# Kernel tuning notes

Hardware: AMD Instinct MI355X
Metric: run time of the kernel (lower is better)

Reference implementation:

```python
import jax, jax.numpy as jnp
import numpy as np

F = 128          # feature_size
N = 512          # num_vertices (batch_size fixed to 1 by the original indexing)
C = 32 * 7 * 7 * 7   # 10976, f2 channel dim
G = 13           # f2 spatial grid (indices = (v+1)*6 in [0,12])
EPS = 1e-5


def _block(x, W1, b1, W2, b2, g, be, m, v):
    # Linear -> ELU -> Linear -> ELU -> Dropout(eval=id) -> BatchNorm1d(eval)
    h = jax.nn.elu(x @ W1 + b1)
    h = jax.nn.elu(h @ W2 + b2)
    return (h - m) * (g * jax.lax.rsqrt(v + EPS)) + be


def setup_inputs() -> dict:
    key = jax.random.key(0)
    ks = iter(jax.random.split(key, 80))

    def nrm(sh, s):
        return jax.random.normal(next(ks), sh, jnp.float32) * s

    def lin(i, o):
        return nrm((i, o), 1.0 / np.sqrt(i)), nrm((o,), 0.01)

    def bn():
        g = 1.0 + nrm((F,), 0.05)
        be = nrm((F,), 0.05)
        m = nrm((F,), 0.1)
        v = jax.random.uniform(next(ks), (F,), jnp.float32) + 0.5
        return g, be, m, v

    d = {}
    d['vertices'] = jax.random.uniform(next(ks), (1, N, 3), jnp.float32) * 2.0 - 1.0
    d['f2'] = nrm((1, G, G, G, C), 0.1)
    ii = jnp.arange(N, dtype=jnp.int32)
    d['v1s_idx'] = jnp.repeat(ii, N)   # edge k=(i,j): i = k//N
    d['v2s_idx'] = jnp.tile(ii, N)     #               j = k%N
    d['adj'] = (jax.random.uniform(next(ks), (N, N)) < 0.05).astype(jnp.float32)

    for p, (i, o) in [('mv', (3, F)), ('mf', (C, F)), ('s1', (2 * F, F)),
                      ('s2', (F, F)), ('s3', (2 * F, F))]:
        W1, b1 = lin(i, o)
        W2, b2 = lin(F, F)
        g, be, m, v = bn()
        d.update({p + '_W1': W1, p + '_b1': b1, p + '_W2': W2, p + '_b2': b2,
                  p + '_g': g, p + '_be': be, p + '_m': m, p + '_v': v})
    W3, b3 = lin(F, 2)
    d['s3_W3'], d['s3_b3'] = W3, b3
    return d


def _forward(vertices, f2, adj,
             mv_W1, mv_b1, mv_W2, mv_b2, mv_g, mv_be, mv_m, mv_v,
             mf_W1, mf_b1, mf_W2, mf_b2, mf_g, mf_be, mf_m, mf_v,
             s1_W1, s1_b1, s1_W2, s1_b2, s1_g, s1_be, s1_m, s1_v,
             s2_W1, s2_b1, s2_W2, s2_b2, s2_g, s2_be, s2_m, s2_v,
             s3_W1, s3_b1, s3_W2, s3_b2, s3_g, s3_be, s3_m, s3_v, s3_W3, s3_b3,
             v1s_idx, v2s_idx):
    b, n, _ = vertices.shape
    flat = vertices.reshape(-1, 3)                        # (B*N, 3)
    idx = ((flat + 1.0) * 6.0).astype(jnp.int32)          # grid indices in [0,12]
    f2e = f2[0, idx[:, 0], idx[:, 1], idx[:, 2], :]       # gather: (B*N, C)
    vf = _block(flat, mv_W1, mv_b1, mv_W2, mv_b2, mv_g, mv_be, mv_m, mv_v)
    ff = _block(f2e, mf_W1, mf_b1, mf_W2, mf_b2, mf_g, mf_be, mf_m, mf_v)
    vert = jnp.concatenate([vf, ff], -1).reshape(b, n, 2 * F)  # (B, N, 2F)

    # stage1: NodeToEdge (endpoint combine) -> MLP block over all N^2 edges
    e1 = vert[:, v1s_idx] + vert[:, v2s_idx]              # (B, N*N, 2F)
    s1 = _block(e1, s1_W1, s1_b1, s1_W2, s1_b2, s1_g, s1_be, s1_m, s1_v)  # (B, E, F)

    # stage2: EdgeToNode (adjacency-masked sum) -> MLP -> NodeToEdge
    nodes = jnp.einsum('bijf,ij->bif', s1.reshape(b, n, n, F), adj)  # (B, N, F)
    n2 = _block(nodes, s2_W1, s2_b1, s2_W2, s2_b2, s2_g, s2_be, s2_m, s2_v)
    s2 = n2[:, v1s_idx] + n2[:, v2s_idx]                  # (B, E, F)

    cat = jnp.concatenate([s1, s2], -1).reshape(b * n * n, 2 * F)
    h = _block(cat, s3_W1, s3_b1, s3_W2, s3_b2, s3_g, s3_be, s3_m, s3_v)
    return (h @ s3_W3 + s3_b3).reshape(b, n, n, 2)


def reference(vertices, f2, v1s_idx, v2s_idx, adj,
              mv_W1, mv_b1, mv_W2, mv_b2, mv_g, mv_be, mv_m, mv_v,
              mf_W1, mf_b1, mf_W2, mf_b2, mf_g, mf_be, mf_m, mf_v,
              s1_W1, s1_b1, s1_W2, s1_b2, s1_g, s1_be, s1_m, s1_v,
              s2_W1, s2_b1, s2_W2, s2_b2, s2_g, s2_be, s2_m, s2_v,
              s3_W1, s3_b1, s3_W2, s3_b2, s3_g, s3_be, s3_m, s3_v, s3_W3, s3_b3):
    return _forward(vertices, f2, adj,
                    mv_W1, mv_b1, mv_W2, mv_b2, mv_g, mv_be, mv_m, mv_v,
                    mf_W1, mf_b1, mf_W2, mf_b2, mf_g, mf_be, mf_m, mf_v,
                    s1_W1, s1_b1, s1_W2, s1_b2, s1_g, s1_be, s1_m, s1_v,
                    s2_W1, s2_b1, s2_W2, s2_b2, s2_g, s2_be, s2_m, s2_v,
                    s3_W1, s3_b1, s3_W2, s3_b2, s3_g, s3_be, s3_m, s3_v, s3_W3, s3_b3,
                    v1s_idx, v2s_idx)
```

## Files before the change

kernel.cpp:

```cpp
#include <hip/hip_runtime.h>
#include <hip/hip_bf16.h>


#define F    128
#define NV   512
#define CCC  10976
#define EPSV 1e-5f

typedef __attribute__((ext_vector_type(8)))  short        short8;
typedef __attribute__((ext_vector_type(4)))  float        f32x4;
typedef __attribute__((ext_vector_type(4)))  float        flt4;
typedef __attribute__((ext_vector_type(4)))  unsigned int u32x4;

union Frag { u32x4 q; short8 s; unsigned int d[4]; unsigned short u[8]; };

__device__ __forceinline__ unsigned short f2bf(float x){
  union { float f; unsigned int u; } c; c.f = x;
  unsigned int r = c.u + 0x7FFFu + ((c.u >> 16) & 1u);
  return (unsigned short)(r >> 16);
}
__device__ __forceinline__ unsigned int pkbf(float a, float b){
  union { __hip_bfloat162 h; unsigned int u; } cv;
  cv.h = __float22bfloat162_rn(make_float2(a, b));
  return cv.u;
}
__device__ __forceinline__ float eluf(float x){
  return x > 0.f ? x : (__expf(x) - 1.f);
}
__device__ __forceinline__ f32x4 mfma16(short8 a, short8 b, f32x4 c){
  return __builtin_amdgcn_mfma_f32_16x16x32_bf16(a, b, c, 0, 0, 0);
}

#define WS_U      0u
#define WS_FFPRE  262144u
#define WS_NODES  524288u
#define WS_WPERM  786432u
#define WS_ADJS   1048576u
#define WS_CNT    1050624u
#define WS_PJ     1052672u
#define WS_VEC    1183744u
#define WS_W2FS1  1188864u
#define WS_W1AFS3 1221632u
#define WS_W2FS3  1254400u
#define WS_W3F    1287168u
#define WS_MFW1F  1291264u
#define WS_END    4101120u
#define WS_PART   4101120u
#define WS_PART_END 15373312u


__global__ __launch_bounds__(256) void k_setup(
    const float* s1W2, const float* s3W1, const float* s3W2, const float* s3W3,
    const float* __restrict__ mfW1,
    const float* s1g, const float* s1be, const float* s1m, const float* s1v,
    const float* s3g, const float* s3be, const float* s3m, const float* s3v,
    const float* s1b2, const float* s3b2, const float* __restrict__ adj,
    unsigned short* w2fs1, unsigned short* w1afs3, unsigned short* w2fs3,
    unsigned short* w3f, unsigned short* __restrict__ mfw1f,
    float* vec, float* zeroreg,
    unsigned short* __restrict__ pj, int* __restrict__ cntI,
    float* __restrict__ cntF)
{
  __shared__ float sm[32 * 132];
  __shared__ unsigned long long msk[8];
  int bid = blockIdx.x, tid = threadIdx.x;

  if (bid < 460){
    int t = bid * 256 + tid;
    if (t < 49152){
      int T = t >> 14, tt = t & 16383;
      int e = tt & 7, lane = (tt >> 3) & 63, grp = tt >> 9;
      int slot = (grp >> 3) * 32 + ((lane >> 4) & 3) * 8 + e;
      int col  = (grp & 7) * 16 + (lane & 15);
      float val;
      unsigned short* dst;
      if (T == 0){ dst = w2fs1; val = s1W2[slot * F + col]; }
      else {
        int kf = (slot & 7) * 16 + (slot >> 3);
        if (T == 1){
          float sc1 = s1g[kf] * rsqrtf(s1v[kf] + EPSV);
          dst = w1afs3; val = sc1 * s3W1[kf * F + col];
        } else {
          dst = w2fs3; val = s3W2[kf * F + col];
        }
      }
      dst[tt] = f2bf(val);
      return;
    }
    t -= 49152;
    if (t < 2048){
      int e = t & 7, lane = (t >> 3) & 63, ks = t >> 9;
      int slot = ks * 32 + ((lane >> 4) & 3) * 8 + e;
      int kf = (slot & 7) * 16 + (slot >> 3);
      int n = lane & 15;
      float sc3 = s3g[kf] * rsqrtf(s3v[kf] + EPSV);
      w3f[t] = f2bf(n < 2 ? sc3 * s3W3[kf * 2 + n] : 0.f);
      return;
    }
    t -= 2048;
    if (t < 1024){
      int f = t & 127, which = t >> 7;
      int s = (f & 15) * 8 + (f >> 4);
      switch (which){
        case 0: vec[512 + s] = s1b2[f]; break;
        case 1: vec[640 + s] = s3b2[f]; break;
        case 2: vec[768 + f] = s1g[f] * rsqrtf(s1v[f] + EPSV); break;
        case 3: vec[896 + f] = s1be[f] - s1m[f] * (s1g[f] * rsqrtf(s1v[f] + EPSV)); break;
        case 4: {
          float a = 0.f;
          for (int k = 0; k < F; ++k){
            float sc = s1g[k] * rsqrtf(s1v[k] + EPSV);
            a = fmaf(s1be[k] - s1m[k] * sc, s3W1[k * F + f], a);
          }
          vec[1024 + f] = a;
        } break;
        case 5: if (f < 16){
          float a = 0.f;
          if (f < 2){
            for (int k = 0; k < F; ++k){
              float sc = s3g[k] * rsqrtf(s3v[k] + EPSV);
              a = fmaf(s3be[k] - s3m[k] * sc, s3W3[k * 2 + f], a);
            }
          }
          vec[1152 + f] = a;
        } break;
        default: break;
      }
      return;
    }
    t -= 1024;
    if (t < 65536) zeroreg[t] = 0.f;
    return;
  }

  if (bid < 803){
    int ksg = bid - 460;
    const float* src = mfW1 + ksg * 32 * F;
    #pragma unroll
    for (int p = 0; p < 4; ++p){
      int g4 = tid + p * 256;
      int row = g4 >> 5, col = (g4 & 31) * 4;
      flt4 v = *(const flt4*)(src + row * F + col);
      *(flt4*)(sm + row * 132 + col) = v;
    }
    __syncthreads();
    unsigned int* dst = (unsigned int*)mfw1f + ksg * 2048;
    #pragma unroll
    for (int q2 = 0; q2 < 8; ++q2){
      int o = (tid * 8 + q2) * 2;
      int nt = o >> 9, lane = (o >> 3) & 63, e = o & 7;
      int k = (lane >> 4) * 8 + e;
      int n = nt * 16 + (lane & 15);
      dst[tid * 8 + q2] = pkbf(sm[k * 132 + n], sm[(k + 1) * 132 + n]);
    }
    return;
  }

  {
    int i = bid - 803, wv = tid >> 6, ln = tid & 63;
    bool p0 = adj[i * NV + tid] != 0.f;
    bool p1 = adj[i * NV + 256 + tid] != 0.f;
    unsigned long long m0 = __ballot(p0);
    unsigned long long m1 = __ballot(p1);
    if (ln == 0){ msk[wv] = m0; msk[4 + wv] = m1; }
    __syncthreads();
    int base0 = 0, base1 = 0, tot = 0;
    #pragma unroll
    for (int g = 0; g < 8; ++g){
      int c = __popcll(msk[g]);
      if (g < wv) base0 += c;
      if (g < 4 + wv) base1 += c;
      tot += c;
    }
    unsigned long long below = (1ull << ln) - 1ull;
    if (p0){
      int r = base0 + __popcll(m0 & below);
      if (r < 128) pj[i * 128 + r] = (unsigned short)tid;
    }
    if (p1){
      int r = base1 + __popcll(m1 & below);
      if (r < 128) pj[i * 128 + r] = (unsigned short)(256 + tid);
    }
    if (tid == 0){ cntI[i] = tot > 128 ? 128 : tot; cntF[i] = (float)tot; }
  }
}

__global__ __launch_bounds__(256) void k_ff1(
    const float* __restrict__ verts, const float* __restrict__ f2,
    const unsigned short* __restrict__ mfw1f, float* __restrict__ ffpre,
    float* __restrict__ partials, int use_parts)
{
  int tid = threadIdx.x, w = tid >> 6, l = tid & 63, g = l >> 4, mm = l & 15;
  int mb = blockIdx.x & 7, kc = blockIdx.x >> 3;
  int v = mb * 64 + w * 16 + mm;
  float x0 = verts[v * 3 + 0], x1 = verts[v * 3 + 1], x2 = verts[v * 3 + 2];
  int i0 = (int)((x0 + 1.f) * 6.f), i1 = (int)((x1 + 1.f) * 6.f), i2 = (int)((x2 + 1.f) * 6.f);
  int base = ((i0 * 13 + i1) * 13 + i2) * CCC;

  f32x4 zero = {0.f, 0.f, 0.f, 0.f};
  f32x4 acc[8];
  #pragma unroll
  for (int nt = 0; nt < 8; ++nt) acc[nt] = zero;

  const u32x4* bt = (const u32x4*)mfw1f;
  #pragma unroll
  for (int kk = 0; kk < 8; ++kk){
    int ksg = kc * 8 + kk;
    if (ksg >= 343) break;
    const float* ap = f2 + base + ksg * 32 + g * 8;
    flt4 a0 = *(const flt4*)ap;
    flt4 a1 = *(const flt4*)(ap + 4);
    Frag a;
    a.d[0] = pkbf(a0.x, a0.y); a.d[1] = pkbf(a0.z, a0.w);
    a.d[2] = pkbf(a1.x, a1.y); a.d[3] = pkbf(a1.z, a1.w);
    #pragma unroll
    for (int nt = 0; nt < 8; ++nt){
      Frag b; b.q = bt[(ksg * 8 + nt) * 64 + l];
      acc[nt] = mfma16(a.s, b.s, acc[nt]);
    }
  }
  if (use_parts){
    #pragma unroll
    for (int nt = 0; nt < 8; ++nt){
      int n = nt * 16 + mm;
      #pragma unroll
      for (int r = 0; r < 4; ++r)
        partials[(kc * NV + mb * 64 + w * 16 + g * 4 + r) * F + n] = acc[nt][r];
    }
  } else {
    #pragma unroll
    for (int nt = 0; nt < 8; ++nt){
      int n = nt * 16 + mm;
      #pragma unroll
      for (int r = 0; r < 4; ++r)
        atomicAdd(&ffpre[(mb * 64 + w * 16 + g * 4 + r) * F + n], acc[nt][r]);
    }
  }
}

__global__ __launch_bounds__(128) void k_vert(
    const float* __restrict__ verts, const float* __restrict__ ffpre,
    const float* __restrict__ partials, int use_parts,
    const float* mvW1, const float* mvb1, const float* mvW2, const float* mvb2,
    const float* mvg, const float* mvbe, const float* mvm, const float* mvv,
    const float* mfb1, const float* mfW2, const float* mfb2,
    const float* mfg, const float* mfbe, const float* mfm, const float* mfv,
    const float* s1W1, const float* s1b1, float* __restrict__ uP)
{
  __shared__ float hv[F], hf[F], vf[F], ff[F];
  int f = threadIdx.x, v = blockIdx.x;
  float x0 = verts[v * 3], x1 = verts[v * 3 + 1], x2 = verts[v * 3 + 2];
  hv[f] = eluf(mvb1[f] + x0 * mvW1[f] + x1 * mvW1[F + f] + x2 * mvW1[2 * F + f]);
  float fp;
  if (use_parts){
    fp = 0.f;
    for (int kc = 0; kc < 43; ++kc) fp += partials[(kc * NV + v) * F + f];
  } else {
    fp = ffpre[v * F + f];
  }
  hf[f] = eluf(fp + mfb1[f]);
  __syncthreads();
  float sv = mvb2[f], sf = mfb2[f];
  for (int k = 0; k < F; ++k){
    sv = fmaf(hv[k], mvW2[k * F + f], sv);
    sf = fmaf(hf[k], mfW2[k * F + f], sf);
  }
  vf[f] = (eluf(sv) - mvm[f]) * (mvg[f] * rsqrtf(mvv[f] + EPSV)) + mvbe[f];
  ff[f] = (eluf(sf) - mfm[f]) * (mfg[f] * rsqrtf(mfv[f] + EPSV)) + mfbe[f];
  __syncthreads();
  float u = 0.5f * s1b1[f];
  for (int k = 0; k < F; ++k){
    u = fmaf(vf[k], s1W1[k * F + f], u);
    u = fmaf(ff[k], s1W1[(128 + k) * F + f], u);
  }
  uP[v * F + f] = u;
}

__global__ __launch_bounds__(256) void k_pass1s(
    const float* __restrict__ uP, const unsigned short* __restrict__ w2fs1,
    const float* __restrict__ vec, const unsigned short* __restrict__ pj,
    const int* __restrict__ cntA, float* __restrict__ nodes)
{
  __shared__ u32x4 Wb[2048];
  __shared__ float ci[F], nblk[F];
  int tid = threadIdx.x, i = blockIdx.x;
  int cnt = cntA[i];
  { const u32x4* ws_ = (const u32x4*)w2fs1;
    #pragma unroll
    for (int ii = 0; ii < 8; ++ii) Wb[tid + 256 * ii] = ws_[tid + 256 * ii]; }
  if (tid < F){ ci[tid] = uP[i * F + tid]; nblk[tid] = 0.f; }
  __syncthreads();

  int w = tid >> 6, l = tid & 63, g = l >> 4, mm = l & 15;
  float b2v[8];
  *(flt4*)&b2v[0] = *(const flt4*)(vec + 512 + mm * 8);
  *(flt4*)&b2v[4] = *(const flt4*)(vec + 516 + mm * 8);

  for (int t = 0; t * 64 < cnt; ++t){
    int row = t * 64 + w * 16 + mm;
    int j = (row < cnt) ? (int)pj[i * 128 + row] : 0;
    f32x4 acc[8];
    #pragma unroll
    for (int nt = 0; nt < 8; ++nt){ float b = b2v[nt]; acc[nt] = (f32x4){b, b, b, b}; }
    #pragma unroll
    for (int ks = 0; ks < 4; ++ks){
      int kb = ks * 32 + g * 8;
      flt4 ua = *(const flt4*)(uP + j * F + kb);
      flt4 ub = *(const flt4*)(uP + j * F + kb + 4);
      flt4 c0 = *(const flt4*)&ci[kb];
      flt4 c1 = *(const flt4*)&ci[kb + 4];
      Frag a;
      a.d[0] = pkbf(eluf(ua.x + c0.x), eluf(ua.y + c0.y));
      a.d[1] = pkbf(eluf(ua.z + c0.z), eluf(ua.w + c0.w));
      a.d[2] = pkbf(eluf(ub.x + c1.x), eluf(ub.y + c1.y));
      a.d[3] = pkbf(eluf(ub.z + c1.z), eluf(ub.w + c1.w));
      #pragma unroll
      for (int nt = 0; nt < 8; ++nt){
        Frag b; b.q = Wb[(ks * 8 + nt) * 64 + l];
        acc[nt] = mfma16(a.s, b.s, acc[nt]);
      }
    }
    int rbase = t * 64 + w * 16 + g * 4;
    float mk[4];
    #pragma unroll
    for (int r = 0; r < 4; ++r) mk[r] = (rbase + r < cnt) ? 1.f : 0.f;
    #pragma unroll
    for (int nt = 0; nt < 8; ++nt){
      float s = mk[0] * eluf(acc[nt][0]);
      s = fmaf(mk[1], eluf(acc[nt][1]), s);
      s = fmaf(mk[2], eluf(acc[nt][2]), s);
      s = fmaf(mk[3], eluf(acc[nt][3]), s);
      s += __shfl_xor(s, 16, 64);
      s += __shfl_xor(s, 32, 64);
      if (l < 16) atomicAdd(&nblk[nt * 16 + mm], s);
    }
  }
  __syncthreads();
  if (tid < F) nodes[i * F + tid] = nblk[tid];
}

__global__ __launch_bounds__(128) void k_mid(
    const float* __restrict__ nodes, const float* __restrict__ cntF,
    const float* __restrict__ vec,
    const float* s2W1, const float* s2b1, const float* s2W2, const float* s2b2,
    const float* s2g, const float* s2be, const float* s2m, const float* s2v,
    const float* s3W1, const float* s3b1, float* __restrict__ wPp)
{
  __shared__ float a[F], b[F];
  int f = threadIdx.x, r = blockIdx.x;
  a[f] = vec[768 + f] * nodes[r * F + f] + vec[896 + f] * cntF[r];
  __syncthreads();
  float s = s2b1[f];
  for (int k = 0; k < F; ++k) s = fmaf(a[k], s2W1[k * F + f], s);
  b[f] = eluf(s);
  __syncthreads();
  float s2 = s2b2[f];
  for (int k = 0; k < F; ++k) s2 = fmaf(b[k], s2W2[k * F + f], s2);
  float n2 = (eluf(s2) - s2m[f]) * (s2g[f] * rsqrtf(s2v[f] + EPSV)) + s2be[f];
  __syncthreads();
  a[f] = n2;
  __syncthreads();
  float wv = 0.5f * (s3b1[f] + vec[1024 + f]);
  for (int k = 0; k < F; ++k) wv = fmaf(a[k], s3W1[(128 + k) * F + f], wv);
  wPp[r * F + ((f & 15) * 8 + (f >> 4))] = wv;
}

__global__ __launch_bounds__(512, 2) void k_pass3(
    const float* __restrict__ uP, const float* __restrict__ wPp,
    const unsigned short* __restrict__ w2fs1, const unsigned short* __restrict__ w1afs3,
    const unsigned short* __restrict__ w2fs3, const unsigned short* __restrict__ w3f,
    const float* __restrict__ vec, const float* __restrict__ s3b3,
    float* __restrict__ out)
{
  __shared__ u32x4 Wall[6144];
  __shared__ __align__(16) char Hb[65536];
  int tid = threadIdx.x;
  {
    const u32x4* p0 = (const u32x4*)w2fs1;
    const u32x4* p1 = (const u32x4*)w1afs3;
    const u32x4* p2 = (const u32x4*)w2fs3;
    #pragma unroll
    for (int ii = 0; ii < 4; ++ii){
      Wall[       tid + 512 * ii] = p0[tid + 512 * ii];
      Wall[2048 + tid + 512 * ii] = p1[tid + 512 * ii];
      Wall[4096 + tid + 512 * ii] = p2[tid + 512 * ii];
    }
  }
  __syncthreads();

  int w = tid >> 6, l = tid & 63, g = l >> 4, mm = l & 15;
  char* hb = Hb + w * 8192;
  int sx = (mm & 7) << 4;

  float b2v1[8], b2v3[8];
  *(flt4*)&b2v1[0] = *(const flt4*)(vec + 512 + mm * 8);
  *(flt4*)&b2v1[4] = *(const flt4*)(vec + 516 + mm * 8);
  *(flt4*)&b2v3[0] = *(const flt4*)(vec + 640 + mm * 8);
  *(flt4*)&b2v3[4] = *(const flt4*)(vec + 644 + mm * 8);
  float bb = (mm < 2) ? (s3b3[mm] + vec[1152 + mm]) : 0.f;

  for (int jb = blockIdx.x * 8 + w; jb < 5120; jb += 2048){
    int tile = jb >> 2, sub = jb & 3;
    int band, idx;
    if (tile < 512)      { band = 0; idx = tile; }
    else if (tile < 896) { band = 1; idx = tile - 512; }
    else if (tile < 1152){ band = 2; idx = tile - 896; }
    else                 { band = 3; idx = tile - 1152; }
    int tpb = 4 - band;
    int i  = band * 128 + idx / tpb;
    int jbase = (band + idx % tpb) * 128 + sub * 32;
    if (jbase + 32 <= i) continue;

    flt4 c0[4], c1[4];
    #pragma unroll
    for (int ks = 0; ks < 4; ++ks){
      c0[ks] = *(const flt4*)(uP + i * F + ks * 32 + g * 8);
      c1[ks] = *(const flt4*)(uP + i * F + ks * 32 + g * 8 + 4);
    }

    f32x4 acc[2][8];
    #pragma unroll
    for (int m = 0; m < 2; ++m)
    #pragma unroll
    for (int nt = 0; nt < 8; ++nt){ float b = b2v1[nt]; acc[m][nt] = (f32x4){b, b, b, b}; }
    #pragma unroll
    for (int ks = 0; ks < 4; ++ks){
      int kb = ks * 32 + g * 8;
      Frag a0, a1;
      {
        const float* p0 = uP + (jbase + mm) * F + kb;
        flt4 ua = *(const flt4*)p0;
        flt4 ub = *(const flt4*)(p0 + 4);
        a0.d[0] = pkbf(eluf(ua.x + c0[ks].x), eluf(ua.y + c0[ks].y));
        a0.d[1] = pkbf(eluf(ua.z + c0[ks].z), eluf(ua.w + c0[ks].w));
        a0.d[2] = pkbf(eluf(ub.x + c1[ks].x), eluf(ub.y + c1[ks].y));
        a0.d[3] = pkbf(eluf(ub.z + c1[ks].z), eluf(ub.w + c1[ks].w));
        const float* p1 = uP + (jbase + 16 + mm) * F + kb;
        flt4 va = *(const flt4*)p1;
        flt4 vb = *(const flt4*)(p1 + 4);
        a1.d[0] = pkbf(eluf(va.x + c0[ks].x), eluf(va.y + c0[ks].y));
        a1.d[1] = pkbf(eluf(va.z + c0[ks].z), eluf(va.w + c0[ks].w));
        a1.d[2] = pkbf(eluf(vb.x + c1[ks].x), eluf(vb.y + c1[ks].y));
        a1.d[3] = pkbf(eluf(vb.z + c1[ks].z), eluf(vb.w + c1[ks].w));
      }
      #pragma unroll
      for (int nt = 0; nt < 8; ++nt){
        Frag b; b.q = Wall[(ks * 8 + nt) * 64 + l];
        acc[0][nt] = mfma16(a0.s, b.s, acc[0][nt]);
        acc[1][nt] = mfma16(a1.s, b.s, acc[1][nt]);
      }
    }
    #pragma unroll
    for (int m = 0; m < 2; ++m)
    #pragma unroll
    for (int r = 0; r < 4; ++r){
      int row = m * 16 + g * 4 + r;
      u32x4 wd;
      #pragma unroll
      for (int q = 0; q < 4; ++q)
        wd[q] = pkbf(eluf(acc[m][2*q][r]), eluf(acc[m][2*q+1][r]));
      *(u32x4*)(hb + row * 256 + ((mm * 16) ^ ((row & 7) << 4))) = wd;
    }

    {
      float wiv[8];
      *(flt4*)&wiv[0] = *(const flt4*)(wPp + i * F + mm * 8);
      *(flt4*)&wiv[4] = *(const flt4*)(wPp + i * F + mm * 8 + 4);
      #pragma unroll
      for (int m = 0; m < 2; ++m)
      #pragma unroll
      for (int nt = 0; nt < 8; ++nt){ float b = wiv[nt]; acc[m][nt] = (f32x4){b, b, b, b}; }
    }
    #pragma unroll
    for (int ks = 0; ks < 4; ++ks){
      Frag a0; a0.q = *(const u32x4*)(hb + mm * 256 + ((ks * 64 + g * 16) ^ sx));
      Frag a1; a1.q = *(const u32x4*)(hb + (16 + mm) * 256 + ((ks * 64 + g * 16) ^ sx));
      #pragma unroll
      for (int nt = 0; nt < 8; ++nt){
        Frag b; b.q = Wall[2048 + (ks * 8 + nt) * 64 + l];
        acc[0][nt] = mfma16(a0.s, b.s, acc[0][nt]);
        acc[1][nt] = mfma16(a1.s, b.s, acc[1][nt]);
      }
    }
    #pragma unroll
    for (int m = 0; m < 2; ++m)
    #pragma unroll
    for (int r = 0; r < 4; ++r){
      int row = m * 16 + g * 4 + r;
      int jj = jbase + row;
      float wjv[8];
      *(flt4*)&wjv[0] = *(const flt4*)(wPp + jj * F + mm * 8);
      *(flt4*)&wjv[4] = *(const flt4*)(wPp + jj * F + mm * 8 + 4);
      u32x4 wd;
      #pragma unroll
      for (int q = 0; q < 4; ++q)
        wd[q] = pkbf(eluf(acc[m][2*q][r] + wjv[2*q]), eluf(acc[m][2*q+1][r] + wjv[2*q+1]));
      *(u32x4*)(hb + row * 256 + ((mm * 16) ^ ((row & 7) << 4))) = wd;
    }

    #pragma unroll
    for (int m = 0; m < 2; ++m)
    #pragma unroll
    for (int nt = 0; nt < 8; ++nt){ float b = b2v3[nt]; acc[m][nt] = (f32x4){b, b, b, b}; }
    #pragma unroll
    for (int ks = 0; ks < 4; ++ks){
      Frag a0; a0.q = *(const u32x4*)(hb + mm * 256 + ((ks * 64 + g * 16) ^ sx));
      Frag a1; a1.q = *(const u32x4*)(hb + (16 + mm) * 256 + ((ks * 64 + g * 16) ^ sx));
      #pragma unroll
      for (int nt = 0; nt < 8; ++nt){
        Frag b; b.q = Wall[4096 + (ks * 8 + nt) * 64 + l];
        acc[0][nt] = mfma16(a0.s, b.s, acc[0][nt]);
        acc[1][nt] = mfma16(a1.s, b.s, acc[1][nt]);
      }
    }
    #pragma unroll
    for (int m = 0; m < 2; ++m)
    #pragma unroll
    for (int r = 0; r < 4; ++r){
      int row = m * 16 + g * 4 + r;
      u32x4 wd;
      #pragma unroll
      for (int q = 0; q < 4; ++q)
        wd[q] = pkbf(eluf(acc[m][2*q][r]), eluf(acc[m][2*q+1][r]));
      *(u32x4*)(hb + row * 256 + ((mm * 16) ^ ((row & 7) << 4))) = wd;
    }

    f32x4 acc4[2] = {{bb, bb, bb, bb}, {bb, bb, bb, bb}};
    {
      const u32x4* w3q = (const u32x4*)w3f;
      #pragma unroll
      for (int ks = 0; ks < 4; ++ks){
        Frag a0; a0.q = *(const u32x4*)(hb + mm * 256 + ((ks * 64 + g * 16) ^ sx));
        Frag a1; a1.q = *(const u32x4*)(hb + (16 + mm) * 256 + ((ks * 64 + g * 16) ^ sx));
        Frag b; b.q = w3q[ks * 64 + l];
        acc4[0] = mfma16(a0.s, b.s, acc4[0]);
        acc4[1] = mfma16(a1.s, b.s, acc4[1]);
      }
    }
    if (mm < 2){
      #pragma unroll
      for (int m = 0; m < 2; ++m)
      #pragma unroll
      for (int r = 0; r < 4; ++r){
        int jr = jbase + m * 16 + g * 4 + r;
        if (jr >= i){
          float val = acc4[m][r];
          out[(i * NV + jr) * 2 + mm] = val;
          out[(jr * NV + i) * 2 + mm] = val;
        }
      }
    }
  }
}

extern "C" void kernel_launch(void* const* d_in, const int* in_sizes, int n_in,
                              void* d_out, int out_size, void* d_ws, size_t ws_size,
                              hipStream_t stream)
{
  (void)in_sizes; (void)n_in; (void)out_size;
  const float* vertices = (const float*)d_in[0];
  const float* f2   = (const float*)d_in[1];
  const float* adj  = (const float*)d_in[4];
  const float* mvW1 = (const float*)d_in[5];
  const float* mvb1 = (const float*)d_in[6];
  const float* mvW2 = (const float*)d_in[7];
  const float* mvb2 = (const float*)d_in[8];
  const float* mvg  = (const float*)d_in[9];
  const float* mvbe = (const float*)d_in[10];
  const float* mvm  = (const float*)d_in[11];
  const float* mvv  = (const float*)d_in[12];
  const float* mfW1 = (const float*)d_in[13];
  const float* mfb1 = (const float*)d_in[14];
  const float* mfW2 = (const float*)d_in[15];
  const float* mfb2 = (const float*)d_in[16];
  const float* mfg  = (const float*)d_in[17];
  const float* mfbe = (const float*)d_in[18];
  const float* mfm  = (const float*)d_in[19];
  const float* mfv  = (const float*)d_in[20];
  const float* s1W1 = (const float*)d_in[21];
  const float* s1b1 = (const float*)d_in[22];
  const float* s1W2 = (const float*)d_in[23];
  const float* s1b2 = (const float*)d_in[24];
  const float* s1g  = (const float*)d_in[25];
  const float* s1be = (const float*)d_in[26];
  const float* s1m  = (const float*)d_in[27];
  const float* s1v  = (const float*)d_in[28];
  const float* s2W1 = (const float*)d_in[29];
  const float* s2b1 = (const float*)d_in[30];
  const float* s2W2 = (const float*)d_in[31];
  const float* s2b2 = (const float*)d_in[32];
  const float* s2g  = (const float*)d_in[33];
  const float* s2be = (const float*)d_in[34];
  const float* s2m  = (const float*)d_in[35];
  const float* s2v  = (const float*)d_in[36];
  const float* s3W1 = (const float*)d_in[37];
  const float* s3b1 = (const float*)d_in[38];
  const float* s3W2 = (const float*)d_in[39];
  const float* s3b2 = (const float*)d_in[40];
  const float* s3g  = (const float*)d_in[41];
  const float* s3be = (const float*)d_in[42];
  const float* s3m  = (const float*)d_in[43];
  const float* s3v  = (const float*)d_in[44];
  const float* s3W3 = (const float*)d_in[45];
  const float* s3b3 = (const float*)d_in[46];

  char* ws = (char*)d_ws;
  float* uP    = (float*)(ws + WS_U);
  float* ffpre = (float*)(ws + WS_FFPRE);
  float* nodes = (float*)(ws + WS_NODES);
  float* wPp   = (float*)(ws + WS_WPERM);
  float* cntF  = (float*)(ws + WS_ADJS);
  int*   cntI  = (int*)(ws + WS_CNT);
  unsigned short* pj = (unsigned short*)(ws + WS_PJ);
  float* vec   = (float*)(ws + WS_VEC);
  unsigned short* w2fs1  = (unsigned short*)(ws + WS_W2FS1);
  unsigned short* w1afs3 = (unsigned short*)(ws + WS_W1AFS3);
  unsigned short* w2fs3  = (unsigned short*)(ws + WS_W2FS3);
  unsigned short* w3f    = (unsigned short*)(ws + WS_W3F);
  unsigned short* mfw1f  = (unsigned short*)(ws + WS_MFW1F);
  float* parts = (float*)(ws + WS_PART);
  int use_parts = (ws_size >= (size_t)WS_PART_END) ? 1 : 0;

  k_setup<<<1315, 256, 0, stream>>>(s1W2, s3W1, s3W2, s3W3, mfW1,
      s1g, s1be, s1m, s1v, s3g, s3be, s3m, s3v, s1b2, s3b2, adj,
      w2fs1, w1afs3, w2fs3, w3f, mfw1f, vec, ffpre, pj, cntI, cntF);
  k_ff1<<<344, 256, 0, stream>>>(vertices, f2, mfw1f, ffpre, parts, use_parts);
  k_vert<<<512, 128, 0, stream>>>(vertices, ffpre, parts, use_parts,
      mvW1, mvb1, mvW2, mvb2, mvg, mvbe, mvm, mvv,
      mfb1, mfW2, mfb2, mfg, mfbe, mfm, mfv,
      s1W1, s1b1, uP);
  k_pass1s<<<512, 256, 0, stream>>>(uP, w2fs1, vec, pj, cntI, nodes);
  k_mid<<<512, 128, 0, stream>>>(nodes, cntF, vec,
      s2W1, s2b1, s2W2, s2b2, s2g, s2be, s2m, s2v, s3W1, s3b1, wPp);
  k_pass3<<<256, 512, 0, stream>>>(uP, wPp, w2fs1, w1afs3, w2fs3, w3f, vec,
      s3b3, (float*)d_out);
}
```

Measured before the change: 111.2 us.

## Fuse adjacency compaction and mid MLP into pass1, add dynamic tile scheduling in pass3

```diff
diff --git a/kernel.cpp b/kernel.cpp
--- a/kernel.cpp
+++ b/kernel.cpp
@@ -33,37 +33,33 @@
 
 #define WS_U      0u
 #define WS_FFPRE  262144u
-#define WS_NODES  524288u
-#define WS_WPERM  786432u
-#define WS_ADJS   1048576u
-#define WS_CNT    1050624u
-#define WS_PJ     1052672u
-#define WS_VEC    1183744u
-#define WS_W2FS1  1188864u
-#define WS_W1AFS3 1221632u
-#define WS_W2FS3  1254400u
-#define WS_W3F    1287168u
-#define WS_MFW1F  1291264u
-#define WS_END    4101120u
-#define WS_PART   4101120u
-#define WS_PART_END 15373312u
+#define WS_WPERM  524288u
+#define WS_CTR    786432u
+#define WS_VEC    787456u
+#define WS_W2FS1  792576u
+#define WS_W1AFS3 825344u
+#define WS_W2FS3  858112u
+#define WS_W3F    890880u
+#define WS_MFW1F  894976u
+#define WS_END    3704832u
+#define WS_PART   3704832u
+#define WS_PART_END 14977024u
 
 
 __global__ __launch_bounds__(256) void k_setup(
     const float* s1W2, const float* s3W1, const float* s3W2, const float* s3W3,
     const float* __restrict__ mfW1,
-    const float* s1g, const float* s1be, const float* s1m, const float* s1v,
+    const float* s1g, const float* s1v,
     const float* s3g, const float* s3be, const float* s3m, const float* s3v,
-    const float* s1b2, const float* s3b2, const float* __restrict__ adj,
+    const float* s1be, const float* s1m,
+    const float* s1b2, const float* s3b2,
     unsigned short* w2fs1, unsigned short* w1afs3, unsigned short* w2fs3,
     unsigned short* w3f, unsigned short* __restrict__ mfw1f,
-    float* vec, float* zeroreg,
-    unsigned short* __restrict__ pj, int* __restrict__ cntI,
-    float* __restrict__ cntF)
+    float* vec, float* zeroreg, unsigned int* ctr, int use_parts)
 {
   __shared__ float sm[32 * 132];
-  __shared__ unsigned long long msk[8];
   int bid = blockIdx.x, tid = threadIdx.x;
+  if (bid == 0 && tid == 0) *ctr = 0u;
 
   if (bid < 460){
     int t = bid * 256 + tid;
@@ -129,11 +125,11 @@
       return;
     }
     t -= 1024;
-    if (t < 65536) zeroreg[t] = 0.f;
+    if (t < 65536 && !use_parts) zeroreg[t] = 0.f;
     return;
   }
 
-  if (bid < 803){
+  {
     int ksg = bid - 460;
     const float* src = mfW1 + ksg * 32 * F;
     #pragma unroll
@@ -153,35 +149,6 @@
       int n = nt * 16 + (lane & 15);
       dst[tid * 8 + q2] = pkbf(sm[k * 132 + n], sm[(k + 1) * 132 + n]);
     }
-    return;
-  }
-
-  {
-    int i = bid - 803, wv = tid >> 6, ln = tid & 63;
-    bool p0 = adj[i * NV + tid] != 0.f;
-    bool p1 = adj[i * NV + 256 + tid] != 0.f;
-    unsigned long long m0 = __ballot(p0);
-    unsigned long long m1 = __ballot(p1);
-    if (ln == 0){ msk[wv] = m0; msk[4 + wv] = m1; }
-    __syncthreads();
-    int base0 = 0, base1 = 0, tot = 0;
-    #pragma unroll
-    for (int g = 0; g < 8; ++g){
-      int c = __popcll(msk[g]);
-      if (g < wv) base0 += c;
-      if (g < 4 + wv) base1 += c;
-      tot += c;
-    }
-    unsigned long long below = (1ull << ln) - 1ull;
-    if (p0){
-      int r = base0 + __popcll(m0 & below);
-      if (r < 128) pj[i * 128 + r] = (unsigned short)tid;
-    }
-    if (p1){
-      int r = base1 + __popcll(m1 & below);
-      if (r < 128) pj[i * 128 + r] = (unsigned short)(256 + tid);
-    }
-    if (tid == 0){ cntI[i] = tot > 128 ? 128 : tot; cntF[i] = (float)tot; }
   }
 }
 
@@ -203,10 +170,9 @@
   for (int nt = 0; nt < 8; ++nt) acc[nt] = zero;
 
   const u32x4* bt = (const u32x4*)mfw1f;
-  #pragma unroll
-  for (int kk = 0; kk < 8; ++kk){
+  int kmax = 343 - kc * 8; if (kmax > 8) kmax = 8;
+  for (int kk = 0; kk < kmax; ++kk){
     int ksg = kc * 8 + kk;
-    if (ksg >= 343) break;
     const float* ap = f2 + base + ksg * 32 + g * 8;
     flt4 a0 = *(const flt4*)ap;
     flt4 a1 = *(const flt4*)(ap + 4);
@@ -238,7 +204,7 @@
   }
 }
 
-__global__ __launch_bounds__(128) void k_vert(
+__global__ __launch_bounds__(256) void k_vert(
     const float* __restrict__ verts, const float* __restrict__ ffpre,
     const float* __restrict__ partials, int use_parts,
     const float* mvW1, const float* mvb1, const float* mvW2, const float* mvb2,
@@ -247,48 +213,98 @@
     const float* mfg, const float* mfbe, const float* mfm, const float* mfv,
     const float* s1W1, const float* s1b1, float* __restrict__ uP)
 {
-  __shared__ float hv[F], hf[F], vf[F], ff[F];
-  int f = threadIdx.x, v = blockIdx.x;
-  float x0 = verts[v * 3], x1 = verts[v * 3 + 1], x2 = verts[v * 3 + 2];
-  hv[f] = eluf(mvb1[f] + x0 * mvW1[f] + x1 * mvW1[F + f] + x2 * mvW1[2 * F + f]);
-  float fp;
-  if (use_parts){
-    fp = 0.f;
-    for (int kc = 0; kc < 43; ++kc) fp += partials[(kc * NV + v) * F + f];
+  __shared__ float hv[F], hf[F], vf[F], ff[F], ph0[F], ph1[F];
+  int tid = threadIdx.x, f = tid & 127, half = tid >> 7, v = blockIdx.x;
+  if (half == 0){
+    float x0 = verts[v * 3], x1 = verts[v * 3 + 1], x2 = verts[v * 3 + 2];
+    hv[f] = eluf(mvb1[f] + x0 * mvW1[f] + x1 * mvW1[F + f] + x2 * mvW1[2 * F + f]);
   } else {
-    fp = ffpre[v * F + f];
-  }
-  hf[f] = eluf(fp + mfb1[f]);
+    float fp;
+    if (use_parts){
+      fp = 0.f;
+      for (int kc = 0; kc < 43; ++kc) fp += partials[(kc * NV + v) * F + f];
+    } else {
+      fp = ffpre[v * F + f];
+    }
+    hf[f] = eluf(fp + mfb1[f]);
+  }
   __syncthreads();
-  float sv = mvb2[f], sf = mfb2[f];
-  for (int k = 0; k < F; ++k){
-    sv = fmaf(hv[k], mvW2[k * F + f], sv);
-    sf = fmaf(hf[k], mfW2[k * F + f], sf);
-  }
-  vf[f] = (eluf(sv) - mvm[f]) * (mvg[f] * rsqrtf(mvv[f] + EPSV)) + mvbe[f];
-  ff[f] = (eluf(sf) - mfm[f]) * (mfg[f] * rsqrtf(mfv[f] + EPSV)) + mfbe[f];
-  __syncthreads();
-  float u = 0.5f * s1b1[f];
-  for (int k = 0; k < F; ++k){
-    u = fmaf(vf[k], s1W1[k * F + f], u);
-    u = fmaf(ff[k], s1W1[(128 + k) * F + f], u);
-  }
-  uP[v * F + f] = u;
-}
-
-__global__ __launch_bounds__(256) void k_pass1s(
+  {
+    float psv = 0.f, psf = 0.f;
+    const float* wv_ = mvW2 + half * 64 * F + f;
+    const float* wf_ = mfW2 + half * 64 * F + f;
+    const float* hvk = hv + half * 64;
+    const float* hfk = hf + half * 64;
+    for (int k = 0; k < 64; ++k){
+      psv = fmaf(hvk[k], wv_[k * F], psv);
+      psf = fmaf(hfk[k], wf_[k * F], psf);
+    }
+    if (half){ ph0[f] = psv; ph1[f] = psf; }
+    __syncthreads();
+    if (!half){
+      float sv = mvb2[f] + psv + ph0[f];
+      float sf = mfb2[f] + psf + ph1[f];
+      vf[f] = (eluf(sv) - mvm[f]) * (mvg[f] * rsqrtf(mvv[f] + EPSV)) + mvbe[f];
+      ff[f] = (eluf(sf) - mfm[f]) * (mfg[f] * rsqrtf(mfv[f] + EPSV)) + mfbe[f];
+    }
+    __syncthreads();
+  }
+  {
+    float pu = 0.f;
+    if (half == 0){
+      for (int k = 0; k < F; ++k) pu = fmaf(vf[k], s1W1[k * F + f], pu);
+    } else {
+      for (int k = 0; k < F; ++k) pu = fmaf(ff[k], s1W1[(128 + k) * F + f], pu);
+    }
+    if (half) ph0[f] = pu;
+    __syncthreads();
+    if (!half) uP[v * F + f] = 0.5f * s1b1[f] + pu + ph0[f];
+  }
+}
+
+__global__ __launch_bounds__(256) void k_pass1m(
     const float* __restrict__ uP, const unsigned short* __restrict__ w2fs1,
-    const float* __restrict__ vec, const unsigned short* __restrict__ pj,
-    const int* __restrict__ cntA, float* __restrict__ nodes)
+    const float* __restrict__ vec, const float* __restrict__ adj,
+    const float* s2W1, const float* s2b1, const float* s2W2, const float* s2b2,
+    const float* s2g, const float* s2be, const float* s2m, const float* s2v,
+    const float* s3W1, const float* s3b1, float* __restrict__ wPp)
 {
   __shared__ u32x4 Wb[2048];
-  __shared__ float ci[F], nblk[F];
+  __shared__ float ci[F], nblk[F], bb[F], mh0[F];
+  __shared__ unsigned short pjl[128];
+  __shared__ unsigned long long msk[8];
   int tid = threadIdx.x, i = blockIdx.x;
-  int cnt = cntA[i];
+  int wv = tid >> 6, ln = tid & 63;
+
+  bool p0 = adj[i * NV + tid] != 0.f;
+  bool p1 = adj[i * NV + 256 + tid] != 0.f;
+  unsigned long long m0 = __ballot(p0);
+  unsigned long long m1 = __ballot(p1);
+  if (ln == 0){ msk[wv] = m0; msk[4 + wv] = m1; }
   { const u32x4* ws_ = (const u32x4*)w2fs1;
     #pragma unroll
     for (int ii = 0; ii < 8; ++ii) Wb[tid + 256 * ii] = ws_[tid + 256 * ii]; }
   if (tid < F){ ci[tid] = uP[i * F + tid]; nblk[tid] = 0.f; }
+  __syncthreads();
+  int base0 = 0, base1 = 0, tot = 0;
+  #pragma unroll
+  for (int g = 0; g < 8; ++g){
+    int c = __popcll(msk[g]);
+    if (g < wv) base0 += c;
+    if (g < 4 + wv) base1 += c;
+    tot += c;
+  }
+  unsigned long long below = (1ull << ln) - 1ull;
+  if (p0){
+    int r = base0 + __popcll(m0 & below);
+    if (r < 128) pjl[r] = (unsigned short)tid;
+  }
+  if (p1){
+    int r = base1 + __popcll(m1 & below);
+    if (r < 128) pjl[r] = (unsigned short)(256 + tid);
+  }
+  int cnt = tot > 128 ? 128 : tot;
+  float cntf = (float)tot;
   __syncthreads();
 
   int w = tid >> 6, l = tid & 63, g = l >> 4, mm = l & 15;
@@ -298,7 +314,7 @@
 
   for (int t = 0; t * 64 < cnt; ++t){
     int row = t * 64 + w * 16 + mm;
-    int j = (row < cnt) ? (int)pj[i * 128 + row] : 0;
+    int j = (row < cnt) ? (int)pjl[row] : 0;
     f32x4 acc[8];
     #pragma unroll
     for (int nt = 0; nt < 8; ++nt){ float b = b2v[nt]; acc[nt] = (f32x4){b, b, b, b}; }
@@ -336,61 +352,63 @@
     }
   }
   __syncthreads();
-  if (tid < F) nodes[i * F + tid] = nblk[tid];
-}
-
-__global__ __launch_bounds__(128) void k_mid(
-    const float* __restrict__ nodes, const float* __restrict__ cntF,
-    const float* __restrict__ vec,
-    const float* s2W1, const float* s2b1, const float* s2W2, const float* s2b2,
-    const float* s2g, const float* s2be, const float* s2m, const float* s2v,
-    const float* s3W1, const float* s3b1, float* __restrict__ wPp)
-{
-  __shared__ float a[F], b[F];
-  int f = threadIdx.x, r = blockIdx.x;
-  a[f] = vec[768 + f] * nodes[r * F + f] + vec[896 + f] * cntF[r];
+
+  if (tid < F) ci[tid] = vec[768 + tid] * nblk[tid] + vec[896 + tid] * cntf;
   __syncthreads();
-  float s = s2b1[f];
-  for (int k = 0; k < F; ++k) s = fmaf(a[k], s2W1[k * F + f], s);
-  b[f] = eluf(s);
-  __syncthreads();
-  float s2 = s2b2[f];
-  for (int k = 0; k < F; ++k) s2 = fmaf(b[k], s2W2[k * F + f], s2);
-  float n2 = (eluf(s2) - s2m[f]) * (s2g[f] * rsqrtf(s2v[f] + EPSV)) + s2be[f];
-  __syncthreads();
-  a[f] = n2;
-  __syncthreads();
-  float wv = 0.5f * (s3b1[f] + vec[1024 + f]);
-  for (int k = 0; k < F; ++k) wv = fmaf(a[k], s3W1[(128 + k) * F + f], wv);
-  wPp[r * F + ((f & 15) * 8 + (f >> 4))] = wv;
-}
-
-__global__ __launch_bounds__(512, 2) void k_pass3(
+  int f = tid & 127, half = tid >> 7;
+  {
+    float p = 0.f;
+    const float* Wc = s2W1 + half * 64 * F + f;
+    const float* av = ci + half * 64;
+    for (int k = 0; k < 64; ++k) p = fmaf(av[k], Wc[k * F], p);
+    if (half) mh0[f] = p;
+    __syncthreads();
+    if (!half) bb[f] = eluf(s2b1[f] + p + mh0[f]);
+    __syncthreads();
+  }
+  {
+    float p = 0.f;
+    const float* Wc = s2W2 + half * 64 * F + f;
+    const float* av = bb + half * 64;
+    for (int k = 0; k < 64; ++k) p = fmaf(av[k], Wc[k * F], p);
+    if (half) mh0[f] = p;
+    __syncthreads();
+    if (!half){
+      float s2 = s2b2[f] + p + mh0[f];
+      nblk[f] = (eluf(s2) - s2m[f]) * (s2g[f] * rsqrtf(s2v[f] + EPSV)) + s2be[f];
+    }
+    __syncthreads();
+  }
+  {
+    float p = 0.f;
+    const float* Wc = s3W1 + (128 + half * 64) * F + f;
+    const float* av = nblk + half * 64;
+    for (int k = 0; k < 64; ++k) p = fmaf(av[k], Wc[k * F], p);
+    if (half) mh0[f] = p;
+    __syncthreads();
+    if (!half){
+      float wvv = 0.5f * (s3b1[f] + vec[1024 + f]) + p + mh0[f];
+      wPp[i * F + ((f & 15) * 8 + (f >> 4))] = wvv;
+    }
+  }
+}
+
+__global__ __launch_bounds__(256, 3) void k_pass3(
     const float* __restrict__ uP, const float* __restrict__ wPp,
     const unsigned short* __restrict__ w2fs1, const unsigned short* __restrict__ w1afs3,
     const unsigned short* __restrict__ w2fs3, const unsigned short* __restrict__ w3f,
     const float* __restrict__ vec, const float* __restrict__ s3b3,
-    float* __restrict__ out)
+    unsigned int* __restrict__ ctr, float* __restrict__ out)
 {
-  __shared__ u32x4 Wall[6144];
-  __shared__ __align__(16) char Hb[65536];
+  __shared__ __align__(16) char Hb[32768];
   int tid = threadIdx.x;
-  {
-    const u32x4* p0 = (const u32x4*)w2fs1;
-    const u32x4* p1 = (const u32x4*)w1afs3;
-    const u32x4* p2 = (const u32x4*)w2fs3;
-    #pragma unroll
-    for (int ii = 0; ii < 4; ++ii){
-      Wall[       tid + 512 * ii] = p0[tid + 512 * ii];
-      Wall[2048 + tid + 512 * ii] = p1[tid + 512 * ii];
-      Wall[4096 + tid + 512 * ii] = p2[tid + 512 * ii];
-    }
-  }
-  __syncthreads();
-
   int w = tid >> 6, l = tid & 63, g = l >> 4, mm = l & 15;
   char* hb = Hb + w * 8192;
   int sx = (mm & 7) << 4;
+
+  const u32x4* B1 = (const u32x4*)w2fs1;
+  const u32x4* B2 = (const u32x4*)w1afs3;
+  const u32x4* B3 = (const u32x4*)w2fs3;
 
   float b2v1[8], b2v3[8];
   *(flt4*)&b2v1[0] = *(const flt4*)(vec + 512 + mm * 8);
@@ -398,8 +416,15 @@
   *(flt4*)&b2v3[0] = *(const flt4*)(vec + 640 + mm * 8);
   *(flt4*)&b2v3[4] = *(const flt4*)(vec + 644 + mm * 8);
   float bb = (mm < 2) ? (s3b3[mm] + vec[1152 + mm]) : 0.f;
-
-  for (int jb = blockIdx.x * 8 + w; jb < 5120; jb += 2048){
+  Frag w3r[4];
+  #pragma unroll
+  for (int ks = 0; ks < 4; ++ks) w3r[ks].q = ((const u32x4*)w3f)[ks * 64 + l];
+
+  for (;;){
+    int jb;
+    if (l == 0) jb = (int)atomicAdd(ctr, 1u);
+    jb = __shfl(jb, 0, 64);
+    if (jb >= 5120) break;
     int tile = jb >> 2, sub = jb & 3;
     int band, idx;
     if (tile < 512)      { band = 0; idx = tile; }
@@ -445,7 +470,7 @@
       }
       #pragma unroll
       for (int nt = 0; nt < 8; ++nt){
-        Frag b; b.q = Wall[(ks * 8 + nt) * 64 + l];
+        Frag b; b.q = B1[(ks * 8 + nt) * 64 + l];
         acc[0][nt] = mfma16(a0.s, b.s, acc[0][nt]);
         acc[1][nt] = mfma16(a1.s, b.s, acc[1][nt]);
       }
@@ -477,7 +502,7 @@
       Frag a1; a1.q = *(const u32x4*)(hb + (16 + mm) * 256 + ((ks * 64 + g * 16) ^ sx));
       #pragma unroll
       for (int nt = 0; nt < 8; ++nt){
-        Frag b; b.q = Wall[2048 + (ks * 8 + nt) * 64 + l];
+        Frag b; b.q = B2[(ks * 8 + nt) * 64 + l];
         acc[0][nt] = mfma16(a0.s, b.s, acc[0][nt]);
         acc[1][nt] = mfma16(a1.s, b.s, acc[1][nt]);
       }
@@ -508,7 +533,7 @@
       Frag a1; a1.q = *(const u32x4*)(hb + (16 + mm) * 256 + ((ks * 64 + g * 16) ^ sx));
       #pragma unroll
       for (int nt = 0; nt < 8; ++nt){
-        Frag b; b.q = Wall[4096 + (ks * 8 + nt) * 64 + l];
+        Frag b; b.q = B3[(ks * 8 + nt) * 64 + l];
         acc[0][nt] = mfma16(a0.s, b.s, acc[0][nt]);
         acc[1][nt] = mfma16(a1.s, b.s, acc[1][nt]);
       }
@@ -526,16 +551,12 @@
     }
 
     f32x4 acc4[2] = {{bb, bb, bb, bb}, {bb, bb, bb, bb}};
-    {
-      const u32x4* w3q = (const u32x4*)w3f;
-      #pragma unroll
-      for (int ks = 0; ks < 4; ++ks){
-        Frag a0; a0.q = *(const u32x4*)(hb + mm * 256 + ((ks * 64 + g * 16) ^ sx));
-        Frag a1; a1.q = *(const u32x4*)(hb + (16 + mm) * 256 + ((ks * 64 + g * 16) ^ sx));
-        Frag b; b.q = w3q[ks * 64 + l];
-        acc4[0] = mfma16(a0.s, b.s, acc4[0]);
-        acc4[1] = mfma16(a1.s, b.s, acc4[1]);
-      }
+    #pragma unroll
+    for (int ks = 0; ks < 4; ++ks){
+      Frag a0; a0.q = *(const u32x4*)(hb + mm * 256 + ((ks * 64 + g * 16) ^ sx));
+      Frag a1; a1.q = *(const u32x4*)(hb + (16 + mm) * 256 + ((ks * 64 + g * 16) ^ sx));
+      acc4[0] = mfma16(a0.s, w3r[ks].s, acc4[0]);
+      acc4[1] = mfma16(a1.s, w3r[ks].s, acc4[1]);
     }
     if (mm < 2){
       #pragma unroll
@@ -607,11 +628,8 @@
   char* ws = (char*)d_ws;
   float* uP    = (float*)(ws + WS_U);
   float* ffpre = (float*)(ws + WS_FFPRE);
-  float* nodes = (float*)(ws + WS_NODES);
   float* wPp   = (float*)(ws + WS_WPERM);
-  float* cntF  = (float*)(ws + WS_ADJS);
-  int*   cntI  = (int*)(ws + WS_CNT);
-  unsigned short* pj = (unsigned short*)(ws + WS_PJ);
+  unsigned int* ctr = (unsigned int*)(ws + WS_CTR);
   float* vec   = (float*)(ws + WS_VEC);
   unsigned short* w2fs1  = (unsigned short*)(ws + WS_W2FS1);
   unsigned short* w1afs3 = (unsigned short*)(ws + WS_W1AFS3);
@@ -621,17 +639,16 @@
   float* parts = (float*)(ws + WS_PART);
   int use_parts = (ws_size >= (size_t)WS_PART_END) ? 1 : 0;
 
-  k_setup<<<1315, 256, 0, stream>>>(s1W2, s3W1, s3W2, s3W3, mfW1,
-      s1g, s1be, s1m, s1v, s3g, s3be, s3m, s3v, s1b2, s3b2, adj,
-      w2fs1, w1afs3, w2fs3, w3f, mfw1f, vec, ffpre, pj, cntI, cntF);
+  k_setup<<<803, 256, 0, stream>>>(s1W2, s3W1, s3W2, s3W3, mfW1,
+      s1g, s1v, s3g, s3be, s3m, s3v, s1be, s1m, s1b2, s3b2,
+      w2fs1, w1afs3, w2fs3, w3f, mfw1f, vec, ffpre, ctr, use_parts);
   k_ff1<<<344, 256, 0, stream>>>(vertices, f2, mfw1f, ffpre, parts, use_parts);
-  k_vert<<<512, 128, 0, stream>>>(vertices, ffpre, parts, use_parts,
+  k_vert<<<512, 256, 0, stream>>>(vertices, ffpre, parts, use_parts,
       mvW1, mvb1, mvW2, mvb2, mvg, mvbe, mvm, mvv,
       mfb1, mfW2, mfb2, mfg, mfbe, mfm, mfv,
       s1W1, s1b1, uP);
-  k_pass1s<<<512, 256, 0, stream>>>(uP, w2fs1, vec, pj, cntI, nodes);
-  k_mid<<<512, 128, 0, stream>>>(nodes, cntF, vec,
+  k_pass1m<<<512, 256, 0, stream>>>(uP, w2fs1, vec, adj,
       s2W1, s2b1, s2W2, s2b2, s2g, s2be, s2m, s2v, s3W1, s3b1, wPp);
-  k_pass3<<<256, 512, 0, stream>>>(uP, wPp, w2fs1, w1afs3, w2fs3, w3f, vec,
-      s3b3, (float*)d_out);
-}
+  k_pass3<<<768, 256, 0, stream>>>(uP, wPp, w2fs1, w1afs3, w2fs3, w3f, vec,
+      s3b3, ctr, (float*)d_out);
+}
```

Result: slower. 222.3 us (+99.9%).
